# Kernel optimization log

Hardware: AMD Instinct MI355X
Metric: run time of the kernel (lower is better)

Reference implementation:

```python
import jax, jax.numpy as jnp
import numpy as np

NUM_NODES = 100000
EMB_DIM = 64
NUM_EDGES = 1280000
NUM_LAYERS = 3


def setup_inputs() -> dict:
    key = jax.random.key(0)
    k1, k2 = jax.random.split(key)
    edge_index = jax.random.randint(k1, (2, NUM_EDGES), 0, NUM_NODES, dtype=jnp.int32)
    emb = jax.random.normal(k2, (NUM_NODES, EMB_DIM), dtype=jnp.float32) * 0.01
    return {"edge_index": edge_index, "emb": emb}


def _lgconv_norm(edge_index):
    # PyG gcn_norm without self-loops: deg over destination nodes,
    # norm_e = deg[src]^-0.5 * deg[dst]^-0.5
    src, dst = edge_index[0], edge_index[1]
    deg = jax.ops.segment_sum(jnp.ones((edge_index.shape[1],), jnp.float32), dst,
                              num_segments=NUM_NODES)
    dinv = jnp.where(deg > 0, jax.lax.rsqrt(jnp.maximum(deg, 1.0)), 0.0)
    return src, dst, dinv[src] * dinv[dst]


def reference(edge_index, emb):
    src, dst, w = _lgconv_norm(edge_index)
    x = emb
    out = x
    for _ in range(NUM_LAYERS):
        # message: gather source embeddings, scale, scatter-add to destination
        x = jax.ops.segment_sum(x[src] * w[:, None], dst, num_segments=NUM_NODES)
        out = out + x
    return out / (NUM_LAYERS + 1)
```

## Files before the change

### kernel.cpp

```cpp
#include <hip/hip_runtime.h>

#define N_NODES 100000
#define EMB 64
#define N_EDGES 1280000
#define N_E4 (N_EDGES / 4)

#define NBUCK 782
#define BUCK_SHIFT 7
#define BUCK_NODES 128
#define NBA 313
#define HTOT (NBUCK * NBA)
#define NBH ((HTOT + 1023) / 1024)

typedef unsigned long long u64;
typedef _Float16 f16;
typedef __attribute__((ext_vector_type(2))) _Float16 f16x2;

__global__ void bucket_hist_kernel(const int* __restrict__ dst, int* __restrict__ hist) {
    __shared__ int lh[NBUCK];
    for (int i = threadIdx.x; i < NBUCK; i += 256) lh[i] = 0;
    __syncthreads();
#pragma unroll
    for (int k = 0; k < 4; ++k) {
        int q = blockIdx.x * 1024 + k * 256 + threadIdx.x;
        if (q < N_E4) {
            int4 d4 = ((const int4*)dst)[q];
            atomicAdd(&lh[d4.x >> BUCK_SHIFT], 1);
            atomicAdd(&lh[d4.y >> BUCK_SHIFT], 1);
            atomicAdd(&lh[d4.z >> BUCK_SHIFT], 1);
            atomicAdd(&lh[d4.w >> BUCK_SHIFT], 1);
        }
    }
    __syncthreads();
    for (int i = threadIdx.x; i < NBUCK; i += 256)
        hist[i * NBA + blockIdx.x] = lh[i];
}

__global__ void hist_scan1_kernel(int* __restrict__ hist, int* __restrict__ hbs) {
    __shared__ int lds[256];
    int base = blockIdx.x * 1024;
    int vals[4];
    int tsum = 0;
#pragma unroll
    for (int k = 0; k < 4; ++k) {
        int i = base + threadIdx.x * 4 + k;
        vals[k] = (i < HTOT) ? hist[i] : 0;
        tsum += vals[k];
    }
    lds[threadIdx.x] = tsum;
    __syncthreads();
    for (int off = 1; off < 256; off <<= 1) {
        int v = (threadIdx.x >= (unsigned)off) ? lds[threadIdx.x - off] : 0;
        __syncthreads();
        lds[threadIdx.x] += v;
        __syncthreads();
    }
    int run = lds[threadIdx.x] - tsum;
    if (threadIdx.x == 255) hbs[blockIdx.x] = lds[255];
    #pragma unroll
    for (int k = 0; k < 4; ++k) {
        int i = base + threadIdx.x * 4 + k;
        if (i < HTOT) hist[i] = run;
        run += vals[k];
    }
}

__global__ void hist_scan2_kernel(int* __restrict__ hbs) {
    __shared__ int lds[256];
    int v = (threadIdx.x < (unsigned)NBH) ? hbs[threadIdx.x] : 0;
    lds[threadIdx.x] = v;
    __syncthreads();
    for (int off = 1; off < 256; off <<= 1) {
        int t = (threadIdx.x >= (unsigned)off) ? lds[threadIdx.x - off] : 0;
        __syncthreads();
        lds[threadIdx.x] += t;
        __syncthreads();
    }
    if (threadIdx.x < (unsigned)NBH) hbs[threadIdx.x] = lds[threadIdx.x] - v;
}

__global__ void bucket_scatter_kernel(const int* __restrict__ src, const int* __restrict__ dst,
                                      const int* __restrict__ hist, const int* __restrict__ hbs,
                                      int* __restrict__ bedge) {
    __shared__ int cur[NBUCK];
    for (int i = threadIdx.x; i < NBUCK; i += 256) {
        int idx = i * NBA + blockIdx.x;
        cur[i] = hist[idx] + hbs[idx >> 10];
    }
    __syncthreads();
#pragma unroll
    for (int k = 0; k < 4; ++k) {
        int q = blockIdx.x * 1024 + k * 256 + threadIdx.x;
        if (q < N_E4) {
            int4 d4 = ((const int4*)dst)[q];
            int4 s4 = ((const int4*)src)[q];
            int p;
            p = atomicAdd(&cur[d4.x >> BUCK_SHIFT], 1);
            bedge[p] = s4.x | ((d4.x & (BUCK_NODES - 1)) << 17);
            p = atomicAdd(&cur[d4.y >> BUCK_SHIFT], 1);
            bedge[p] = s4.y | ((d4.y & (BUCK_NODES - 1)) << 17);
            p = atomicAdd(&cur[d4.z >> BUCK_SHIFT], 1);
            bedge[p] = s4.z | ((d4.z & (BUCK_NODES - 1)) << 17);
            p = atomicAdd(&cur[d4.w >> BUCK_SHIFT], 1);
            bedge[p] = s4.w | ((d4.w & (BUCK_NODES - 1)) << 17);
        }
    }
}

__global__ void bucket_build_kernel(const int* __restrict__ hist, const int* __restrict__ hbs,
                                    const int* __restrict__ bedge, const float* __restrict__ emb,
                                    int* __restrict__ col, int* __restrict__ row_start,
                                    float* __restrict__ dinv, float* __restrict__ rdinv,
                                    f16* __restrict__ y0) {
    __shared__ int lh[BUCK_NODES];
    __shared__ int sc[256];
    __shared__ int cur[BUCK_NODES];
    int k = blockIdx.x;
    int tid = threadIdx.x;
    int i0 = k * NBA;
    int beg = hist[i0] + hbs[i0 >> 10];
    int end;
    if (k + 1 < NBUCK) {
        int i1 = (k + 1) * NBA;
        end = hist[i1] + hbs[i1 >> 10];
    } else {
        end = N_EDGES;
    }
    if (tid < BUCK_NODES) lh[tid] = 0;
    __syncthreads();
    for (int i = beg + tid; i < end; i += 256)
        atomicAdd(&lh[((unsigned)bedge[i]) >> 17], 1);
    __syncthreads();
    int own = (tid < BUCK_NODES) ? lh[tid] : 0;
    sc[tid] = own;
    __syncthreads();
    for (int off = 1; off < 256; off <<= 1) {
        int v = (tid >= off) ? sc[tid - off] : 0;
        __syncthreads();
        sc[tid] += v;
        __syncthreads();
    }
    if (tid < BUCK_NODES) cur[tid] = sc[tid] - own;
    __syncthreads();
    if (tid < BUCK_NODES) {
        int node = k * BUCK_NODES + tid;
        if (node <= N_NODES) {
            row_start[node] = beg + cur[tid];
            if (node < N_NODES) {
                int d = lh[tid];
                float fd = (float)d;
                dinv[node]  = (d > 0) ? rsqrtf(fd) : 0.0f;
                rdinv[node] = (d > 0) ? sqrtf(fd) : 0.0f;
            }
        }
    }
    __syncthreads();
    for (int i = beg + tid; i < end; i += 256) {
        unsigned pe = (unsigned)bedge[i];
        int r = atomicAdd(&cur[pe >> 17], 1);
        col[beg + r] = (int)(pe & 0x1FFFFu);
    }
    int nbase = k * BUCK_NODES;
#pragma unroll
    for (int it = 0; it < (BUCK_NODES * 16) / 256; ++it) {
        int i = it * 256 + tid;
        int node = nbase + (i >> 4);
        if (node < N_NODES) {
            float dd = (float)lh[i >> 4];
            float dv = (dd > 0.0f) ? rsqrtf(dd) : 0.0f;
            int quad = i & 15;
            float4 v = ((const float4*)emb)[(size_t)node * 16 + quad];
            f16 h[4] = {(f16)(v.x * dv), (f16)(v.y * dv), (f16)(v.z * dv), (f16)(v.w * dv)};
            ((u64*)y0)[(size_t)node * 16 + quad] = *(const u64*)h;
        }
    }
}

template <bool FINAL>
__global__ void gather_kernel(const int* __restrict__ row_start, const int* __restrict__ col,
                              const float* __restrict__ dinv, const float* __restrict__ rdinv,
                              const f16* __restrict__ yin, f16* __restrict__ yout,
                              const float* __restrict__ emb,
                              const f16* __restrict__ y1, const f16* __restrict__ y2,
                              float* __restrict__ out) {
    unsigned int gid = blockIdx.x * blockDim.x + threadIdx.x;
    unsigned int row = gid >> 6;
    int lane = (int)(gid & 63u);
    int s = lane >> 5;
    int j = lane & 31;
    if (row >= N_NODES) return;
    int beg = row_start[row];
    int end = row_start[row + 1];
    const f16* yj = yin + 2 * j;
    float accx = 0.0f, accy = 0.0f;
    for (int cb = beg; cb < end; cb += 64) {
        int idx = cb + lane;
        int ci = 0;
        if (idx < end) ci = col[idx];
        int n = end - cb;
        if (n > 64) n = 64;
        int kk = 0;
        for (; kk + 8 <= n; kk += 8) {
            int c0 = __shfl(ci, kk + s);
            int c1 = __shfl(ci, kk + s + 2);
            int c2 = __shfl(ci, kk + s + 4);
            int c3 = __shfl(ci, kk + s + 6);
            unsigned u0 = *(const unsigned*)(yj + (unsigned)c0 * EMB);
            unsigned u1 = *(const unsigned*)(yj + (unsigned)c1 * EMB);
            unsigned u2 = *(const unsigned*)(yj + (unsigned)c2 * EMB);
            unsigned u3 = *(const unsigned*)(yj + (unsigned)c3 * EMB);
            f16x2 h0 = __builtin_bit_cast(f16x2, u0);
            f16x2 h1 = __builtin_bit_cast(f16x2, u1);
            f16x2 h2 = __builtin_bit_cast(f16x2, u2);
            f16x2 h3 = __builtin_bit_cast(f16x2, u3);
            accx += (float)h0.x + (float)h1.x + (float)h2.x + (float)h3.x;
            accy += (float)h0.y + (float)h1.y + (float)h2.y + (float)h3.y;
        }
        if (kk + 4 <= n) {
            int c0 = __shfl(ci, kk + s);
            int c1 = __shfl(ci, kk + s + 2);
            unsigned u0 = *(const unsigned*)(yj + (unsigned)c0 * EMB);
            unsigned u1 = *(const unsigned*)(yj + (unsigned)c1 * EMB);
            f16x2 h0 = __builtin_bit_cast(f16x2, u0);
            f16x2 h1 = __builtin_bit_cast(f16x2, u1);
            accx += (float)h0.x + (float)h1.x;
            accy += (float)h0.y + (float)h1.y;
            kk += 4;
        }
        for (; kk < n; ++kk) {
            int c = __shfl(ci, kk);
            if (s == (kk & 1)) {
                unsigned u = *(const unsigned*)(yj + (unsigned)c * EMB);
                f16x2 h = __builtin_bit_cast(f16x2, u);
                accx += (float)h.x;
                accy += (float)h.y;
            }
        }
    }
    accx += __shfl_xor(accx, 32);
    accy += __shfl_xor(accy, 32);
    if (s == 0) {
        float dv = dinv[row];
        unsigned int o = row * EMB + 2 * (unsigned)j;
        if (!FINAL) {
            float sc = dv * dv;
            f16x2 h;
            h.x = (f16)(accx * sc);
            h.y = (f16)(accy * sc);
            *(unsigned*)(yout + o) = __builtin_bit_cast(unsigned, h);
        } else {
            float rv = rdinv[row];
            float2 e2 = *(const float2*)(emb + o);
            f16x2 a = __builtin_bit_cast(f16x2, *(const unsigned*)(y1 + o));
            f16x2 b = __builtin_bit_cast(f16x2, *(const unsigned*)(y2 + o));
            float rx = 0.25f * (e2.x + rv * ((float)a.x + (float)b.x) + dv * accx);
            float ry = 0.25f * (e2.y + rv * ((float)a.y + (float)b.y) + dv * accy);
            __builtin_nontemporal_store(rx, out + o);
            __builtin_nontemporal_store(ry, out + o + 1);
        }
    }
}

extern "C" void kernel_launch(void* const* d_in, const int* in_sizes, int n_in,
                              void* d_out, int out_size, void* d_ws, size_t ws_size,
                              hipStream_t stream) {
    const int*   edge = (const int*)d_in[0];
    const int*   src  = edge;
    const int*   dst  = edge + N_EDGES;
    const float* emb  = (const float*)d_in[1];
    float*       out  = (float*)d_out;

    char* ws = (char*)d_ws;
    size_t off = 0;
    int* row_start = (int*)(ws + off); off += 400016;
    int* hbs       = (int*)(ws + off); off += 1024;
    float* dinv    = (float*)(ws + off); off += 400000;
    float* rdinv   = (float*)(ws + off); off += 400000;
    int* hist      = (int*)(ws + off); off += (size_t)HTOT * 4 + 16;
    int* col       = (int*)(ws + off); off += (size_t)N_EDGES * 4;
    f16* y0        = (f16*)(ws + off); off += (size_t)N_NODES * EMB * 2;
    f16* y1        = (f16*)(ws + off); off += (size_t)N_NODES * EMB * 2;
    f16* y2        = (f16*)(ws + off); off += (size_t)N_NODES * EMB * 2;

    int* bedge = (int*)y1;

    bucket_hist_kernel<<<NBA, 256, 0, stream>>>(dst, hist);
    hist_scan1_kernel<<<NBH, 256, 0, stream>>>(hist, hbs);
    hist_scan2_kernel<<<1, 256, 0, stream>>>(hbs);
    bucket_scatter_kernel<<<NBA, 256, 0, stream>>>(src, dst, hist, hbs, bedge);
    bucket_build_kernel<<<NBUCK, 256, 0, stream>>>(hist, hbs, bedge, emb, col,
                                                   row_start, dinv, rdinv, y0);

    const unsigned int gthreads = (unsigned int)N_NODES * EMB;
    const int gblocks = (int)((gthreads + 255) / 256);
    gather_kernel<false><<<gblocks, 256, 0, stream>>>(row_start, col, dinv, rdinv,
                                                      y0, y1, emb, y1, y2, out);
    gather_kernel<false><<<gblocks, 256, 0, stream>>>(row_start, col, dinv, rdinv,
                                                      y1, y2, emb, y1, y2, out);
    gather_kernel<true><<<gblocks, 256, 0, stream>>>(row_start, col, dinv, rdinv,
                                                     y2, (f16*)0, emb, y1, y2, out);
}
```

Baseline: 259.2 us.

## Replace per-block bucket histogram scan with global atomic bucket cursors

The two-level scan over a per-block bucket histogram is replaced by a global per-bucket total (built with atomics), a single-block scan, and per-block slot reservation through atomicAdd on global bucket cursors inside the scatter kernel. This removes one scan kernel and the large per-block histogram traffic, and shortens the build kernel's range lookup. In exchange the edge order within a bucket becomes nondeterministic, and it adds a memset plus global atomic contention on the bucket cursors.

Result: slower. 270.1 us (+4.2%).

```diff
diff --git a/kernel.cpp b/kernel.cpp
--- a/kernel.cpp
+++ b/kernel.cpp
@@ -9,14 +9,12 @@
 #define BUCK_SHIFT 7
 #define BUCK_NODES 128
 #define NBA 313
-#define HTOT (NBUCK * NBA)
-#define NBH ((HTOT + 1023) / 1024)
 
 typedef unsigned long long u64;
 typedef _Float16 f16;
 typedef __attribute__((ext_vector_type(2))) _Float16 f16x2;
 
-__global__ void bucket_hist_kernel(const int* __restrict__ dst, int* __restrict__ hist) {
+__global__ void hist_total_kernel(const int* __restrict__ dst, int* __restrict__ gdeg) {
     __shared__ int lh[NBUCK];
     for (int i = threadIdx.x; i < NBUCK; i += 256) lh[i] = 0;
     __syncthreads();
@@ -33,81 +31,90 @@
     }
     __syncthreads();
     for (int i = threadIdx.x; i < NBUCK; i += 256)
-        hist[i * NBA + blockIdx.x] = lh[i];
-}
-
-__global__ void hist_scan1_kernel(int* __restrict__ hist, int* __restrict__ hbs) {
-    __shared__ int lds[256];
-    int base = blockIdx.x * 1024;
+        if (lh[i]) atomicAdd(&gdeg[i], lh[i]);
+}
+
+__global__ void base_scan_kernel(const int* __restrict__ gdeg, int* __restrict__ gbase,
+                                 int* __restrict__ gcur) {
+    __shared__ int sc[256];
+    int tid = threadIdx.x;
     int vals[4];
     int tsum = 0;
 #pragma unroll
     for (int k = 0; k < 4; ++k) {
-        int i = base + threadIdx.x * 4 + k;
-        vals[k] = (i < HTOT) ? hist[i] : 0;
+        int i = tid * 4 + k;
+        vals[k] = (i < NBUCK) ? gdeg[i] : 0;
         tsum += vals[k];
     }
-    lds[threadIdx.x] = tsum;
+    sc[tid] = tsum;
     __syncthreads();
     for (int off = 1; off < 256; off <<= 1) {
-        int v = (threadIdx.x >= (unsigned)off) ? lds[threadIdx.x - off] : 0;
+        int v = (tid >= off) ? sc[tid - off] : 0;
         __syncthreads();
-        lds[threadIdx.x] += v;
+        sc[tid] += v;
         __syncthreads();
     }
-    int run = lds[threadIdx.x] - tsum;
-    if (threadIdx.x == 255) hbs[blockIdx.x] = lds[255];
-    #pragma unroll
+    int run = sc[tid] - tsum;
+#pragma unroll
     for (int k = 0; k < 4; ++k) {
-        int i = base + threadIdx.x * 4 + k;
-        if (i < HTOT) hist[i] = run;
-        run += vals[k];
-    }
-}
-
-__global__ void hist_scan2_kernel(int* __restrict__ hbs) {
-    __shared__ int lds[256];
-    int v = (threadIdx.x < (unsigned)NBH) ? hbs[threadIdx.x] : 0;
-    lds[threadIdx.x] = v;
-    __syncthreads();
-    for (int off = 1; off < 256; off <<= 1) {
-        int t = (threadIdx.x >= (unsigned)off) ? lds[threadIdx.x - off] : 0;
-        __syncthreads();
-        lds[threadIdx.x] += t;
-        __syncthreads();
-    }
-    if (threadIdx.x < (unsigned)NBH) hbs[threadIdx.x] = lds[threadIdx.x] - v;
+        int i = tid * 4 + k;
+        if (i < NBUCK) {
+            gbase[i] = run;
+            gcur[i]  = run;
+            run += vals[k];
+        }
+    }
+    if (tid == 255) gbase[NBUCK] = N_EDGES;
 }
 
 __global__ void bucket_scatter_kernel(const int* __restrict__ src, const int* __restrict__ dst,
-                                      const int* __restrict__ hist, const int* __restrict__ hbs,
-                                      int* __restrict__ bedge) {
-    __shared__ int cur[NBUCK];
-    for (int i = threadIdx.x; i < NBUCK; i += 256) {
-        int idx = i * NBA + blockIdx.x;
-        cur[i] = hist[idx] + hbs[idx >> 10];
-    }
-    __syncthreads();
+                                      int* __restrict__ gcur, int* __restrict__ bedge) {
+    __shared__ int cnt[NBUCK];
+    const int b = blockIdx.x;
+    const int tid = threadIdx.x;
+    for (int i = tid; i < NBUCK; i += 256) cnt[i] = 0;
+    __syncthreads();
+
+    unsigned pk[16];
+    int bk[16];
 #pragma unroll
     for (int k = 0; k < 4; ++k) {
-        int q = blockIdx.x * 1024 + k * 256 + threadIdx.x;
+        int q = b * 1024 + k * 256 + tid;
         if (q < N_E4) {
             int4 d4 = ((const int4*)dst)[q];
             int4 s4 = ((const int4*)src)[q];
-            int p;
-            p = atomicAdd(&cur[d4.x >> BUCK_SHIFT], 1);
-            bedge[p] = s4.x | ((d4.x & (BUCK_NODES - 1)) << 17);
-            p = atomicAdd(&cur[d4.y >> BUCK_SHIFT], 1);
-            bedge[p] = s4.y | ((d4.y & (BUCK_NODES - 1)) << 17);
-            p = atomicAdd(&cur[d4.z >> BUCK_SHIFT], 1);
-            bedge[p] = s4.z | ((d4.z & (BUCK_NODES - 1)) << 17);
-            p = atomicAdd(&cur[d4.w >> BUCK_SHIFT], 1);
-            bedge[p] = s4.w | ((d4.w & (BUCK_NODES - 1)) << 17);
-        }
-    }
-}
-
-__global__ void bucket_build_kernel(const int* __restrict__ hist, const int* __restrict__ hbs,
+            pk[4*k+0] = (unsigned)(s4.x | ((d4.x & (BUCK_NODES - 1)) << 17));
+            pk[4*k+1] = (unsigned)(s4.y | ((d4.y & (BUCK_NODES - 1)) << 17));
+            pk[4*k+2] = (unsigned)(s4.z | ((d4.z & (BUCK_NODES - 1)) << 17));
+            pk[4*k+3] = (unsigned)(s4.w | ((d4.w & (BUCK_NODES - 1)) << 17));
+            bk[4*k+0] = d4.x >> BUCK_SHIFT;
+            bk[4*k+1] = d4.y >> BUCK_SHIFT;
+            bk[4*k+2] = d4.z >> BUCK_SHIFT;
+            bk[4*k+3] = d4.w >> BUCK_SHIFT;
+            atomicAdd(&cnt[bk[4*k+0]], 1);
+            atomicAdd(&cnt[bk[4*k+1]], 1);
+            atomicAdd(&cnt[bk[4*k+2]], 1);
+            atomicAdd(&cnt[bk[4*k+3]], 1);
+        } else {
+            bk[4*k+0] = -1; bk[4*k+1] = -1; bk[4*k+2] = -1; bk[4*k+3] = -1;
+        }
+    }
+    __syncthreads();
+    for (int i = tid; i < NBUCK; i += 256) {
+        int c = cnt[i];
+        cnt[i] = c ? atomicAdd(&gcur[i], c) : 0;
+    }
+    __syncthreads();
+#pragma unroll
+    for (int e = 0; e < 16; ++e) {
+        if (bk[e] >= 0) {
+            int slot = atomicAdd(&cnt[bk[e]], 1);
+            bedge[slot] = (int)pk[e];
+        }
+    }
+}
+
+__global__ void bucket_build_kernel(const int* __restrict__ gbase,
                                     const int* __restrict__ bedge, const float* __restrict__ emb,
                                     int* __restrict__ col, int* __restrict__ row_start,
                                     float* __restrict__ dinv, float* __restrict__ rdinv,
@@ -117,15 +124,8 @@
     __shared__ int cur[BUCK_NODES];
     int k = blockIdx.x;
     int tid = threadIdx.x;
-    int i0 = k * NBA;
-    int beg = hist[i0] + hbs[i0 >> 10];
-    int end;
-    if (k + 1 < NBUCK) {
-        int i1 = (k + 1) * NBA;
-        end = hist[i1] + hbs[i1 >> 10];
-    } else {
-        end = N_EDGES;
-    }
+    int beg = gbase[k];
+    int end = gbase[k + 1];
     if (tid < BUCK_NODES) lh[tid] = 0;
     __syncthreads();
     for (int i = beg + tid; i < end; i += 256)
@@ -273,10 +273,11 @@
     char* ws = (char*)d_ws;
     size_t off = 0;
     int* row_start = (int*)(ws + off); off += 400016;
-    int* hbs       = (int*)(ws + off); off += 1024;
+    int* gdeg      = (int*)(ws + off); off += 3136;
+    int* gbase     = (int*)(ws + off); off += 3136;
+    int* gcur      = (int*)(ws + off); off += 3136;
     float* dinv    = (float*)(ws + off); off += 400000;
     float* rdinv   = (float*)(ws + off); off += 400000;
-    int* hist      = (int*)(ws + off); off += (size_t)HTOT * 4 + 16;
     int* col       = (int*)(ws + off); off += (size_t)N_EDGES * 4;
     f16* y0        = (f16*)(ws + off); off += (size_t)N_NODES * EMB * 2;
     f16* y1        = (f16*)(ws + off); off += (size_t)N_NODES * EMB * 2;
@@ -284,11 +285,11 @@
 
     int* bedge = (int*)y1;
 
-    bucket_hist_kernel<<<NBA, 256, 0, stream>>>(dst, hist);
-    hist_scan1_kernel<<<NBH, 256, 0, stream>>>(hist, hbs);
-    hist_scan2_kernel<<<1, 256, 0, stream>>>(hbs);
-    bucket_scatter_kernel<<<NBA, 256, 0, stream>>>(src, dst, hist, hbs, bedge);
-    bucket_build_kernel<<<NBUCK, 256, 0, stream>>>(hist, hbs, bedge, emb, col,
+    hipMemsetAsync(gdeg, 0, (size_t)NBUCK * sizeof(int), stream);
+    hist_total_kernel<<<NBA, 256, 0, stream>>>(dst, gdeg);
+    base_scan_kernel<<<1, 256, 0, stream>>>(gdeg, gbase, gcur);
+    bucket_scatter_kernel<<<NBA, 256, 0, stream>>>(src, dst, gcur, bedge);
+    bucket_build_kernel<<<NBUCK, 256, 0, stream>>>(gbase, bedge, emb, col,
                                                    row_start, dinv, rdinv, y0);
 
     const unsigned int gthreads = (unsigned int)N_NODES * EMB;
```

## Split f16 embeddings into column slices and gather per slice with 8-lane groups

Applied to the files above, without the earlier changes.

Stores the intermediate f16 embedding tables as four 16-column slices, so each slice (3.2 MB) can stay cache-resident. The gather kernel assigns blocks a slice and a node half by block index, and uses 8-lane groups per row, each loading 8 neighbours at once. The goal is to cut L2/MALL misses on random neighbour gathers by shrinking the working set each gather touches. The cost is that col and row_start are re-read four times, one per slice, and there are more shuffles per edge.

After: 295.4 us. +14.0%, slower.

```diff
diff --git a/kernel.cpp b/kernel.cpp
--- a/kernel.cpp
+++ b/kernel.cpp
@@ -4,6 +4,7 @@
 #define EMB 64
 #define N_EDGES 1280000
 #define N_E4 (N_EDGES / 4)
+#define SLICE_F16 (N_NODES * 16)
 
 #define NBUCK 782
 #define BUCK_SHIFT 7
@@ -15,6 +16,7 @@
 typedef unsigned long long u64;
 typedef _Float16 f16;
 typedef __attribute__((ext_vector_type(2))) _Float16 f16x2;
+typedef __attribute__((ext_vector_type(2))) float f32x2;
 
 __global__ void bucket_hist_kernel(const int* __restrict__ dst, int* __restrict__ hist) {
     __shared__ int lh[NBUCK];
@@ -168,10 +170,13 @@
         if (node < N_NODES) {
             float dd = (float)lh[i >> 4];
             float dv = (dd > 0.0f) ? rsqrtf(dd) : 0.0f;
-            int quad = i & 15;
-            float4 v = ((const float4*)emb)[(size_t)node * 16 + quad];
+            int q16 = i & 15;
+            int slice = q16 >> 2;
+            int qs = q16 & 3;
+            float4 v = ((const float4*)emb)[(size_t)node * 16 + q16];
             f16 h[4] = {(f16)(v.x * dv), (f16)(v.y * dv), (f16)(v.z * dv), (f16)(v.w * dv)};
-            ((u64*)y0)[(size_t)node * 16 + quad] = *(const u64*)h;
+            *(u64*)(y0 + (size_t)slice * SLICE_F16 + (size_t)node * 16 + qs * 4) =
+                *(const u64*)h;
         }
     }
 }
@@ -183,81 +188,70 @@
                               const float* __restrict__ emb,
                               const f16* __restrict__ y1, const f16* __restrict__ y2,
                               float* __restrict__ out) {
-    unsigned int gid = blockIdx.x * blockDim.x + threadIdx.x;
-    unsigned int row = gid >> 6;
-    int lane = (int)(gid & 63u);
-    int s = lane >> 5;
-    int j = lane & 31;
-    if (row >= N_NODES) return;
-    int beg = row_start[row];
-    int end = row_start[row + 1];
-    const f16* yj = yin + 2 * j;
-    float accx = 0.0f, accy = 0.0f;
-    for (int cb = beg; cb < end; cb += 64) {
-        int idx = cb + lane;
+    unsigned b = blockIdx.x;
+    int role = b & 7;
+    int k = role >> 1;
+    int half = role & 1;
+    int w = threadIdx.x >> 6;
+    int lane = (int)(threadIdx.x & 63u);
+    int g = lane >> 3;
+    int j = lane & 7;
+    unsigned row = (unsigned)(half * (N_NODES / 2) + (b >> 3) * 32 + w * 8 + g);
+    unsigned limit = (unsigned)((half + 1) * (N_NODES / 2));
+    if (row >= limit) return;
+    int beg = __builtin_nontemporal_load(row_start + row);
+    int end = __builtin_nontemporal_load(row_start + (row + 1));
+    const f16* tab = yin + (size_t)k * SLICE_F16 + 2 * j;
+    float ax = 0.0f, ay = 0.0f;
+    for (int cb = beg; cb < end; cb += 8) {
+        int idx = cb + j;
         int ci = 0;
-        if (idx < end) ci = col[idx];
+        if (idx < end) ci = __builtin_nontemporal_load(col + idx);
         int n = end - cb;
-        if (n > 64) n = 64;
-        int kk = 0;
-        for (; kk + 8 <= n; kk += 8) {
-            int c0 = __shfl(ci, kk + s);
-            int c1 = __shfl(ci, kk + s + 2);
-            int c2 = __shfl(ci, kk + s + 4);
-            int c3 = __shfl(ci, kk + s + 6);
-            unsigned u0 = *(const unsigned*)(yj + (unsigned)c0 * EMB);
-            unsigned u1 = *(const unsigned*)(yj + (unsigned)c1 * EMB);
-            unsigned u2 = *(const unsigned*)(yj + (unsigned)c2 * EMB);
-            unsigned u3 = *(const unsigned*)(yj + (unsigned)c3 * EMB);
-            f16x2 h0 = __builtin_bit_cast(f16x2, u0);
-            f16x2 h1 = __builtin_bit_cast(f16x2, u1);
-            f16x2 h2 = __builtin_bit_cast(f16x2, u2);
-            f16x2 h3 = __builtin_bit_cast(f16x2, u3);
-            accx += (float)h0.x + (float)h1.x + (float)h2.x + (float)h3.x;
-            accy += (float)h0.y + (float)h1.y + (float)h2.y + (float)h3.y;
-        }
-        if (kk + 4 <= n) {
-            int c0 = __shfl(ci, kk + s);
-            int c1 = __shfl(ci, kk + s + 2);
-            unsigned u0 = *(const unsigned*)(yj + (unsigned)c0 * EMB);
-            unsigned u1 = *(const unsigned*)(yj + (unsigned)c1 * EMB);
-            f16x2 h0 = __builtin_bit_cast(f16x2, u0);
-            f16x2 h1 = __builtin_bit_cast(f16x2, u1);
-            accx += (float)h0.x + (float)h1.x;
-            accy += (float)h0.y + (float)h1.y;
-            kk += 4;
-        }
-        for (; kk < n; ++kk) {
-            int c = __shfl(ci, kk);
-            if (s == (kk & 1)) {
-                unsigned u = *(const unsigned*)(yj + (unsigned)c * EMB);
-                f16x2 h = __builtin_bit_cast(f16x2, u);
-                accx += (float)h.x;
-                accy += (float)h.y;
-            }
-        }
-    }
-    accx += __shfl_xor(accx, 32);
-    accy += __shfl_xor(accy, 32);
-    if (s == 0) {
-        float dv = dinv[row];
-        unsigned int o = row * EMB + 2 * (unsigned)j;
-        if (!FINAL) {
-            float sc = dv * dv;
-            f16x2 h;
-            h.x = (f16)(accx * sc);
-            h.y = (f16)(accy * sc);
-            *(unsigned*)(yout + o) = __builtin_bit_cast(unsigned, h);
-        } else {
-            float rv = rdinv[row];
-            float2 e2 = *(const float2*)(emb + o);
-            f16x2 a = __builtin_bit_cast(f16x2, *(const unsigned*)(y1 + o));
-            f16x2 b = __builtin_bit_cast(f16x2, *(const unsigned*)(y2 + o));
-            float rx = 0.25f * (e2.x + rv * ((float)a.x + (float)b.x) + dv * accx);
-            float ry = 0.25f * (e2.y + rv * ((float)a.y + (float)b.y) + dv * accy);
-            __builtin_nontemporal_store(rx, out + o);
-            __builtin_nontemporal_store(ry, out + o + 1);
-        }
+        if (n > 8) n = 8;
+        int c0 = __shfl(ci, 0, 8), c1 = __shfl(ci, 1, 8);
+        int c2 = __shfl(ci, 2, 8), c3 = __shfl(ci, 3, 8);
+        int c4 = __shfl(ci, 4, 8), c5 = __shfl(ci, 5, 8);
+        int c6 = __shfl(ci, 6, 8), c7 = __shfl(ci, 7, 8);
+        unsigned u0 = *(const unsigned*)(tab + (unsigned)c0 * 16);
+        unsigned u1 = *(const unsigned*)(tab + (unsigned)c1 * 16);
+        unsigned u2 = *(const unsigned*)(tab + (unsigned)c2 * 16);
+        unsigned u3 = *(const unsigned*)(tab + (unsigned)c3 * 16);
+        unsigned u4 = *(const unsigned*)(tab + (unsigned)c4 * 16);
+        unsigned u5 = *(const unsigned*)(tab + (unsigned)c5 * 16);
+        unsigned u6 = *(const unsigned*)(tab + (unsigned)c6 * 16);
+        unsigned u7 = *(const unsigned*)(tab + (unsigned)c7 * 16);
+        f16x2 h;
+        h = __builtin_bit_cast(f16x2, u0);            { ax += (float)h.x; ay += (float)h.y; }
+        h = __builtin_bit_cast(f16x2, u1); if (n > 1) { ax += (float)h.x; ay += (float)h.y; }
+        h = __builtin_bit_cast(f16x2, u2); if (n > 2) { ax += (float)h.x; ay += (float)h.y; }
+        h = __builtin_bit_cast(f16x2, u3); if (n > 3) { ax += (float)h.x; ay += (float)h.y; }
+        h = __builtin_bit_cast(f16x2, u4); if (n > 4) { ax += (float)h.x; ay += (float)h.y; }
+        h = __builtin_bit_cast(f16x2, u5); if (n > 5) { ax += (float)h.x; ay += (float)h.y; }
+        h = __builtin_bit_cast(f16x2, u6); if (n > 6) { ax += (float)h.x; ay += (float)h.y; }
+        h = __builtin_bit_cast(f16x2, u7); if (n > 7) { ax += (float)h.x; ay += (float)h.y; }
+    }
+    float dv = __builtin_nontemporal_load(dinv + row);
+    unsigned so = (unsigned)k * SLICE_F16 + row * 16u + 2u * (unsigned)j;
+    if (!FINAL) {
+        float scale = dv * dv;
+        f16x2 h;
+        h.x = (f16)(ax * scale);
+        h.y = (f16)(ay * scale);
+        unsigned hv = __builtin_bit_cast(unsigned, h);
+        __builtin_nontemporal_store(hv, (unsigned*)(yout + so));
+    } else {
+        float rv = __builtin_nontemporal_load(rdinv + row);
+        unsigned od = row * EMB + (unsigned)k * 16u + 2u * (unsigned)j;
+        f32x2 e2 = __builtin_nontemporal_load((const f32x2*)(emb + od));
+        unsigned ua = __builtin_nontemporal_load((const unsigned*)(y1 + so));
+        unsigned ub = __builtin_nontemporal_load((const unsigned*)(y2 + so));
+        f16x2 a = __builtin_bit_cast(f16x2, ua);
+        f16x2 bb = __builtin_bit_cast(f16x2, ub);
+        f32x2 r;
+        r.x = 0.25f * (e2.x + rv * ((float)a.x + (float)bb.x) + dv * ax);
+        r.y = 0.25f * (e2.y + rv * ((float)a.y + (float)bb.y) + dv * ay);
+        __builtin_nontemporal_store(r, (f32x2*)(out + od));
     }
 }
 
@@ -291,8 +285,7 @@
     bucket_build_kernel<<<NBUCK, 256, 0, stream>>>(hist, hbs, bedge, emb, col,
                                                    row_start, dinv, rdinv, y0);
 
-    const unsigned int gthreads = (unsigned int)N_NODES * EMB;
-    const int gblocks = (int)((gthreads + 255) / 256);
+    const int gblocks = 8 * ((N_NODES / 2 + 31) / 32);
     gather_kernel<false><<<gblocks, 256, 0, stream>>>(row_start, col, dinv, rdinv,
                                                       y0, y1, emb, y1, y2, out);
     gather_kernel<false><<<gblocks, 256, 0, stream>>>(row_start, col, dinv, rdinv,
```

## Widen bucket-sort grid and fold block-sum scan into consumer kernels

Applied to the files above, without the earlier changes.

The histogram and scatter kernels now use 1250 blocks, each handling 1024 edges (one int4 per thread), instead of 313 blocks each looping four times. This raises parallelism in the preprocessing passes. The first-level scan now processes 4096 entries per block, and the separate second-level scan launch is removed. Its small prefix over block sums is recomputed redundantly inside the scatter and build kernels, and the larger histogram is placed in the y2 buffer. This trades one launch and a serial pass for duplicated tiny scans and a histogram four times larger.

Result: slower. 271.9 us (+4.9%).

```diff
diff --git a/kernel.cpp b/kernel.cpp
--- a/kernel.cpp
+++ b/kernel.cpp
@@ -8,9 +8,10 @@
 #define NBUCK 782
 #define BUCK_SHIFT 7
 #define BUCK_NODES 128
-#define NBA 313
+#define NBA 1250
 #define HTOT (NBUCK * NBA)
-#define NBH ((HTOT + 1023) / 1024)
+#define SC1 4096
+#define NBH ((HTOT + SC1 - 1) / SC1)
 
 typedef unsigned long long u64;
 typedef _Float16 f16;
@@ -20,17 +21,12 @@
     __shared__ int lh[NBUCK];
     for (int i = threadIdx.x; i < NBUCK; i += 256) lh[i] = 0;
     __syncthreads();
-#pragma unroll
-    for (int k = 0; k < 4; ++k) {
-        int q = blockIdx.x * 1024 + k * 256 + threadIdx.x;
-        if (q < N_E4) {
-            int4 d4 = ((const int4*)dst)[q];
-            atomicAdd(&lh[d4.x >> BUCK_SHIFT], 1);
-            atomicAdd(&lh[d4.y >> BUCK_SHIFT], 1);
-            atomicAdd(&lh[d4.z >> BUCK_SHIFT], 1);
-            atomicAdd(&lh[d4.w >> BUCK_SHIFT], 1);
-        }
-    }
+    int q = blockIdx.x * 256 + threadIdx.x;
+    int4 d4 = ((const int4*)dst)[q];
+    atomicAdd(&lh[d4.x >> BUCK_SHIFT], 1);
+    atomicAdd(&lh[d4.y >> BUCK_SHIFT], 1);
+    atomicAdd(&lh[d4.z >> BUCK_SHIFT], 1);
+    atomicAdd(&lh[d4.w >> BUCK_SHIFT], 1);
     __syncthreads();
     for (int i = threadIdx.x; i < NBUCK; i += 256)
         hist[i * NBA + blockIdx.x] = lh[i];
@@ -38,12 +34,12 @@
 
 __global__ void hist_scan1_kernel(int* __restrict__ hist, int* __restrict__ hbs) {
     __shared__ int lds[256];
-    int base = blockIdx.x * 1024;
-    int vals[4];
+    int base = blockIdx.x * SC1;
+    int vals[16];
     int tsum = 0;
 #pragma unroll
-    for (int k = 0; k < 4; ++k) {
-        int i = base + threadIdx.x * 4 + k;
+    for (int k = 0; k < 16; ++k) {
+        int i = base + threadIdx.x * 16 + k;
         vals[k] = (i < HTOT) ? hist[i] : 0;
         tsum += vals[k];
     }
@@ -57,54 +53,50 @@
     }
     int run = lds[threadIdx.x] - tsum;
     if (threadIdx.x == 255) hbs[blockIdx.x] = lds[255];
-    #pragma unroll
-    for (int k = 0; k < 4; ++k) {
-        int i = base + threadIdx.x * 4 + k;
+#pragma unroll
+    for (int k = 0; k < 16; ++k) {
+        int i = base + threadIdx.x * 16 + k;
         if (i < HTOT) hist[i] = run;
         run += vals[k];
     }
-}
-
-__global__ void hist_scan2_kernel(int* __restrict__ hbs) {
-    __shared__ int lds[256];
-    int v = (threadIdx.x < (unsigned)NBH) ? hbs[threadIdx.x] : 0;
-    lds[threadIdx.x] = v;
-    __syncthreads();
-    for (int off = 1; off < 256; off <<= 1) {
-        int t = (threadIdx.x >= (unsigned)off) ? lds[threadIdx.x - off] : 0;
-        __syncthreads();
-        lds[threadIdx.x] += t;
-        __syncthreads();
-    }
-    if (threadIdx.x < (unsigned)NBH) hbs[threadIdx.x] = lds[threadIdx.x] - v;
 }
 
 __global__ void bucket_scatter_kernel(const int* __restrict__ src, const int* __restrict__ dst,
                                       const int* __restrict__ hist, const int* __restrict__ hbs,
                                       int* __restrict__ bedge) {
     __shared__ int cur[NBUCK];
-    for (int i = threadIdx.x; i < NBUCK; i += 256) {
-        int idx = i * NBA + blockIdx.x;
-        cur[i] = hist[idx] + hbs[idx >> 10];
-    }
-    __syncthreads();
-#pragma unroll
-    for (int k = 0; k < 4; ++k) {
-        int q = blockIdx.x * 1024 + k * 256 + threadIdx.x;
-        if (q < N_E4) {
-            int4 d4 = ((const int4*)dst)[q];
-            int4 s4 = ((const int4*)src)[q];
-            int p;
-            p = atomicAdd(&cur[d4.x >> BUCK_SHIFT], 1);
-            bedge[p] = s4.x | ((d4.x & (BUCK_NODES - 1)) << 17);
-            p = atomicAdd(&cur[d4.y >> BUCK_SHIFT], 1);
-            bedge[p] = s4.y | ((d4.y & (BUCK_NODES - 1)) << 17);
-            p = atomicAdd(&cur[d4.z >> BUCK_SHIFT], 1);
-            bedge[p] = s4.z | ((d4.z & (BUCK_NODES - 1)) << 17);
-            p = atomicAdd(&cur[d4.w >> BUCK_SHIFT], 1);
-            bedge[p] = s4.w | ((d4.w & (BUCK_NODES - 1)) << 17);
-        }
-    }
+    __shared__ int hbx[NBH];
+    __shared__ int ssc[256];
+    const int tid = threadIdx.x;
+    const int b = blockIdx.x;
+    int v = (tid < NBH) ? hbs[tid] : 0;
+    ssc[tid] = v;
+    __syncthreads();
+    for (int off = 1; off < 256; off <<= 1) {
+        int t = (tid >= off) ? ssc[tid - off] : 0;
+        __syncthreads();
+        ssc[tid] += t;
+        __syncthreads();
+    }
+    if (tid < NBH) hbx[tid] = ssc[tid] - v;
+    __syncthreads();
+    for (int i = tid; i < NBUCK; i += 256) {
+        int idx = i * NBA + b;
+        cur[i] = hist[idx] + hbx[idx >> 12];
+    }
+    __syncthreads();
+    int q = b * 256 + tid;
+    int4 d4 = ((const int4*)dst)[q];
+    int4 s4 = ((const int4*)src)[q];
+    int p;
+    p = atomicAdd(&cur[d4.x >> BUCK_SHIFT], 1);
+    bedge[p] = s4.x | ((d4.x & (BUCK_NODES - 1)) << 17);
+    p = atomicAdd(&cur[d4.y >> BUCK_SHIFT], 1);
+    bedge[p] = s4.y | ((d4.y & (BUCK_NODES - 1)) << 17);
+    p = atomicAdd(&cur[d4.z >> BUCK_SHIFT], 1);
+    bedge[p] = s4.z | ((d4.z & (BUCK_NODES - 1)) << 17);
+    p = atomicAdd(&cur[d4.w >> BUCK_SHIFT], 1);
+    bedge[p] = s4.w | ((d4.w & (BUCK_NODES - 1)) << 17);
 }
 
 __global__ void bucket_build_kernel(const int* __restrict__ hist, const int* __restrict__ hbs,
@@ -115,19 +107,30 @@
     __shared__ int lh[BUCK_NODES];
     __shared__ int sc[256];
     __shared__ int cur[BUCK_NODES];
+    __shared__ int hbx[NBH];
     int k = blockIdx.x;
     int tid = threadIdx.x;
+    int v = (tid < NBH) ? hbs[tid] : 0;
+    sc[tid] = v;
+    __syncthreads();
+    for (int off = 1; off < 256; off <<= 1) {
+        int t = (tid >= off) ? sc[tid - off] : 0;
+        __syncthreads();
+        sc[tid] += t;
+        __syncthreads();
+    }
+    if (tid < NBH) hbx[tid] = sc[tid] - v;
+    if (tid < BUCK_NODES) lh[tid] = 0;
+    __syncthreads();
     int i0 = k * NBA;
-    int beg = hist[i0] + hbs[i0 >> 10];
+    int beg = hist[i0] + hbx[i0 >> 12];
     int end;
     if (k + 1 < NBUCK) {
         int i1 = (k + 1) * NBA;
-        end = hist[i1] + hbs[i1 >> 10];
+        end = hist[i1] + hbx[i1 >> 12];
     } else {
         end = N_EDGES;
     }
-    if (tid < BUCK_NODES) lh[tid] = 0;
-    __syncthreads();
     for (int i = beg + tid; i < end; i += 256)
         atomicAdd(&lh[((unsigned)bedge[i]) >> 17], 1);
     __syncthreads();
@@ -135,9 +138,9 @@
     sc[tid] = own;
     __syncthreads();
     for (int off = 1; off < 256; off <<= 1) {
-        int v = (tid >= off) ? sc[tid - off] : 0;
-        __syncthreads();
-        sc[tid] += v;
+        int t = (tid >= off) ? sc[tid - off] : 0;
+        __syncthreads();
+        sc[tid] += t;
         __syncthreads();
     }
     if (tid < BUCK_NODES) cur[tid] = sc[tid] - own;
@@ -169,8 +172,8 @@
             float dd = (float)lh[i >> 4];
             float dv = (dd > 0.0f) ? rsqrtf(dd) : 0.0f;
             int quad = i & 15;
-            float4 v = ((const float4*)emb)[(size_t)node * 16 + quad];
-            f16 h[4] = {(f16)(v.x * dv), (f16)(v.y * dv), (f16)(v.z * dv), (f16)(v.w * dv)};
+            float4 vv = ((const float4*)emb)[(size_t)node * 16 + quad];
+            f16 h[4] = {(f16)(vv.x * dv), (f16)(vv.y * dv), (f16)(vv.z * dv), (f16)(vv.w * dv)};
             ((u64*)y0)[(size_t)node * 16 + quad] = *(const u64*)h;
         }
     }
@@ -276,17 +279,16 @@
     int* hbs       = (int*)(ws + off); off += 1024;
     float* dinv    = (float*)(ws + off); off += 400000;
     float* rdinv   = (float*)(ws + off); off += 400000;
-    int* hist      = (int*)(ws + off); off += (size_t)HTOT * 4 + 16;
     int* col       = (int*)(ws + off); off += (size_t)N_EDGES * 4;
     f16* y0        = (f16*)(ws + off); off += (size_t)N_NODES * EMB * 2;
     f16* y1        = (f16*)(ws + off); off += (size_t)N_NODES * EMB * 2;
     f16* y2        = (f16*)(ws + off); off += (size_t)N_NODES * EMB * 2;
 
     int* bedge = (int*)y1;
+    int* hist  = (int*)y2;
 
     bucket_hist_kernel<<<NBA, 256, 0, stream>>>(dst, hist);
     hist_scan1_kernel<<<NBH, 256, 0, stream>>>(hist, hbs);
-    hist_scan2_kernel<<<1, 256, 0, stream>>>(hbs);
     bucket_scatter_kernel<<<NBA, 256, 0, stream>>>(src, dst, hist, hbs, bedge);
     bucket_build_kernel<<<NBUCK, 256, 0, stream>>>(hist, hbs, bedge, emb, col,
                                                    row_start, dinv, rdinv, y0);
```
